# Kernel optimization log

Hardware: AMD Instinct MI355X
Metric: run time of the kernel (lower is better)

The kernel has to match this reference:

```python
import jax, jax.numpy as jnp
import numpy as np

# RT-DETR matcher hyperparameters (from config)
ALPHA, GAMMA = 0.25, 2.0
C_CLASS, C_BBOX, C_GIOU = 2.0, 5.0, 2.0
B, Q, C, T = 32, 300, 80, 100  # batch, queries, classes, targets-per-image


def _center_to_corners(b):
    cx, cy, w, h = jnp.split(b, 4, axis=-1)
    return jnp.concatenate([cx - 0.5 * w, cy - 0.5 * h, cx + 0.5 * w, cy + 0.5 * h], axis=-1)


def _generalized_box_iou(boxes1, boxes2):
    # boxes1 [N,4], boxes2 [M,4] in corner format -> [N,M] GIoU
    area1 = (boxes1[:, 2] - boxes1[:, 0]) * (boxes1[:, 3] - boxes1[:, 1])
    area2 = (boxes2[:, 2] - boxes2[:, 0]) * (boxes2[:, 3] - boxes2[:, 1])
    lt = jnp.maximum(boxes1[:, None, :2], boxes2[None, :, :2])
    rb = jnp.minimum(boxes1[:, None, 2:], boxes2[None, :, 2:])
    wh = jnp.clip(rb - lt, 0.0)
    inter = wh[..., 0] * wh[..., 1]
    union = area1[:, None] + area2[None, :] - inter
    iou = inter / union
    lt_e = jnp.minimum(boxes1[:, None, :2], boxes2[None, :, :2])
    rb_e = jnp.maximum(boxes1[:, None, 2:], boxes2[None, :, 2:])
    wh_e = jnp.clip(rb_e - lt_e, 0.0)
    enclose = wh_e[..., 0] * wh_e[..., 1]
    return iou - (enclose - union) / enclose


def setup_inputs() -> dict:
    key = jax.random.key(0)
    k1, k2, k3, k4 = jax.random.split(key, 4)
    logits = jax.random.normal(k1, (B, Q, C), dtype=jnp.float32)
    pred_boxes = jax.random.uniform(k2, (B, Q, 4), dtype=jnp.float32)
    target_labels = jax.random.randint(k3, (B * T,), 0, C)
    target_boxes = jax.random.uniform(k4, (B * T, 4), dtype=jnp.float32)
    return {"logits": logits, "pred_boxes": pred_boxes,
            "target_labels": target_labels, "target_boxes": target_boxes}


def reference(logits, pred_boxes, target_labels, target_boxes):
    batch_size, num_queries, num_classes = logits.shape
    out_bbox = pred_boxes.reshape(-1, 4)                      # [B*Q, 4]
    # focal-style class cost (use_focal_loss=True)
    out_prob = jax.nn.sigmoid(logits.reshape(-1, num_classes))  # [B*Q, C]
    out_prob = out_prob[:, target_labels]                       # [B*Q, B*T]
    neg_cost = (1 - ALPHA) * out_prob ** GAMMA * -jnp.log(1 - out_prob + 1e-8)
    pos_cost = ALPHA * (1 - out_prob) ** GAMMA * -jnp.log(out_prob + 1e-8)
    class_cost = pos_cost - neg_cost
    # pairwise L1 cost on cxcywh boxes
    bbox_cost = jnp.sum(jnp.abs(out_bbox[:, None, :] - target_boxes[None, :, :]), axis=-1)
    # pairwise GIoU cost on corner boxes
    giou_cost = -_generalized_box_iou(_center_to_corners(out_bbox), _center_to_corners(target_boxes))
    cost_matrix = C_BBOX * bbox_cost + C_CLASS * class_cost + C_GIOU * giou_cost
    return cost_matrix.reshape(batch_size, num_queries, -1)    # [B, Q, B*T]
```

## Files before the change

kernel.cpp:

```cpp
#include <hip/hip_runtime.h>


constexpr int BB = 32, QQ = 300, CN = 80, TT = 100;
constexpr int NQ = BB * QQ;
constexpr int NT = BB * TT;
constexpr int JQ = NT / 4;

__global__ __launch_bounds__(256) void class_cost_kernel(
    const float* __restrict__ logits, float* __restrict__ cc2, int n) {
  int idx = blockIdx.x * blockDim.x + threadIdx.x;
  if (idx >= n) return;
  float x = logits[idx];
  float p = 1.0f / (1.0f + expf(-x));
  float neg = 0.75f * p * p * (-logf(1.0f - p + 1e-8f));
  float pos = 0.25f * (1.0f - p) * (1.0f - p) * (-logf(p + 1e-8f));
  cc2[idx] = 2.0f * (pos - neg);
}

template <bool USE_TABLE>
__global__ __launch_bounds__(256) void pair_kernel(
    const float4* __restrict__ pred_boxes,
    const float4* __restrict__ target_boxes,
    const int4*   __restrict__ labels4,
    const float*  __restrict__ cc2,
    const float*  __restrict__ logits,
    float4*       __restrict__ out)
{
  int tid = blockIdx.x * blockDim.x + threadIdx.x;
  if (tid >= NQ * JQ) return;
  int i  = tid / JQ;
  int jq = tid - i * JQ;

  float4 p = pred_boxes[i];
  float px0 = p.x - 0.5f * p.z, py0 = p.y - 0.5f * p.w;
  float px1 = p.x + 0.5f * p.z, py1 = p.y + 0.5f * p.w;
  float pa  = (px1 - px0) * (py1 - py0);

  int4 lab = labels4[jq];
  const int* labp = &lab.x;
  const float* ccrow = USE_TABLE ? (cc2 + i * CN) : nullptr;
  const float* lgrow = USE_TABLE ? nullptr : (logits + i * CN);

  float res[4];
#pragma unroll
  for (int k = 0; k < 4; ++k) {
    float4 t = target_boxes[jq * 4 + k];
    float l1 = fabsf(p.x - t.x) + fabsf(p.y - t.y) +
               fabsf(p.z - t.z) + fabsf(p.w - t.w);
    float tx0 = t.x - 0.5f * t.z, ty0 = t.y - 0.5f * t.w;
    float tx1 = t.x + 0.5f * t.z, ty1 = t.y + 0.5f * t.w;
    float ta  = (tx1 - tx0) * (ty1 - ty0);
    float ltx = fmaxf(px0, tx0), lty = fmaxf(py0, ty0);
    float rbx = fminf(px1, tx1), rby = fminf(py1, ty1);
    float iw = fmaxf(rbx - ltx, 0.0f), ih = fmaxf(rby - lty, 0.0f);
    float inter = iw * ih;
    float uni = pa + ta - inter;
    float iou = inter / uni;
    float ex0 = fminf(px0, tx0), ey0 = fminf(py0, ty0);
    float ex1 = fmaxf(px1, tx1), ey1 = fmaxf(py1, ty1);
    float ew = fmaxf(ex1 - ex0, 0.0f), eh = fmaxf(ey1 - ey0, 0.0f);
    float enc = ew * eh;
    float giou = iou - (enc - uni) / enc;

    int l = labp[k];
    float cls;
    if (USE_TABLE) {
      cls = ccrow[l];
    } else {
      float x = lgrow[l];
      float pr = 1.0f / (1.0f + expf(-x));
      float neg = 0.75f * pr * pr * (-logf(1.0f - pr + 1e-8f));
      float pos = 0.25f * (1.0f - pr) * (1.0f - pr) * (-logf(pr + 1e-8f));
      cls = 2.0f * (pos - neg);
    }
    res[k] = 5.0f * l1 + cls - 2.0f * giou;
  }
  out[tid] = make_float4(res[0], res[1], res[2], res[3]);
}

extern "C" void kernel_launch(void* const* d_in, const int* in_sizes, int n_in,
                              void* d_out, int out_size, void* d_ws, size_t ws_size,
                              hipStream_t stream) {
  const float*  logits = (const float*)d_in[0];
  const float4* pred   = (const float4*)d_in[1];
  const int4*   labels = (const int4*)d_in[2];
  const float4* tboxes = (const float4*)d_in[3];
  float4* out = (float4*)d_out;

  size_t need = (size_t)NQ * CN * sizeof(float);
  int pair_threads = NQ * JQ;
  int pair_blocks = (pair_threads + 255) / 256;

  if (ws_size >= need) {
    float* cc2 = (float*)d_ws;
    int n = NQ * CN;
    class_cost_kernel<<<(n + 255) / 256, 256, 0, stream>>>(logits, cc2, n);
    pair_kernel<true><<<pair_blocks, 256, 0, stream>>>(
        pred, tboxes, labels, cc2, logits, out);
  } else {
    pair_kernel<false><<<pair_blocks, 256, 0, stream>>>(
        pred, tboxes, labels, nullptr, logits, out);
  }
}
```

Baseline: 171.7 us.

## Tile pair kernel over 32-row chunks, keep target data in registers, use fast reciprocals

Restructures the pair kernel onto a 2D grid. Each thread owns four targets, precomputes their corners, areas and labels once, then loops over 32 prediction rows staged in shared memory. This removes the per-element integer divide and the repeated target loads and corner math. It also replaces the IEEE divisions with the hardware approximate reciprocal and drops the clamp on the enclosing width and height. That changes numerics slightly, and the grid is small (4 stripes by 300 row chunks), which may limit occupancy.

```diff
diff --git a/kernel.cpp b/kernel.cpp
--- a/kernel.cpp
+++ b/kernel.cpp
@@ -4,7 +4,9 @@
 constexpr int BB = 32, QQ = 300, CN = 80, TT = 100;
 constexpr int NQ = BB * QQ;
 constexpr int NT = BB * TT;
-constexpr int JQ = NT / 4;
+constexpr int JG = NT / 4;
+constexpr int RCHUNK = 32;
+constexpr int STRIPES = (JG + 255) / 256;
 
 __global__ __launch_bounds__(256) void class_cost_kernel(
     const float* __restrict__ logits, float* __restrict__ cc2, int n) {
@@ -17,65 +19,126 @@
   cc2[idx] = 2.0f * (pos - neg);
 }
 
-template <bool USE_TABLE>
-__global__ __launch_bounds__(256) void pair_kernel(
+__global__ __launch_bounds__(256, 4) void pair_kernel(
     const float4* __restrict__ pred_boxes,
     const float4* __restrict__ target_boxes,
-    const int4*   __restrict__ labels4,
+    const int*    __restrict__ labels,
     const float*  __restrict__ cc2,
+    float4*       __restrict__ out)
+{
+  const int tid  = threadIdx.x;
+  const int jg   = blockIdx.x * 256 + tid;
+  const int row0 = blockIdx.y * RCHUNK;
+
+  __shared__ float4 s_pred[RCHUNK];
+  if (tid < RCHUNK) s_pred[tid] = pred_boxes[row0 + tid];
+  __syncthreads();
+  if (jg >= JG) return;
+
+  float tcx[4], tcy[4], tw[4], th[4];
+  float tx0[4], ty0[4], tx1[4], ty1[4], ta[4];
+  int   loff[4];
+#pragma unroll
+  for (int k = 0; k < 4; ++k) {
+    float4 t = target_boxes[jg * 4 + k];
+    tcx[k] = t.x; tcy[k] = t.y; tw[k] = t.z; th[k] = t.w;
+    tx0[k] = t.x - 0.5f * t.z;  ty0[k] = t.y - 0.5f * t.w;
+    tx1[k] = t.x + 0.5f * t.z;  ty1[k] = t.y + 0.5f * t.w;
+    ta[k]  = (tx1[k] - tx0[k]) * (ty1[k] - ty0[k]);
+    loff[k] = labels[jg * 4 + k];
+  }
+
+  const size_t outbase = (size_t)jg;
+  for (int r = 0; r < RCHUNK; ++r) {
+    const int i = row0 + r;
+    float4 p = s_pred[r];
+    float px0 = p.x - 0.5f * p.z, py0 = p.y - 0.5f * p.w;
+    float px1 = p.x + 0.5f * p.z, py1 = p.y + 0.5f * p.w;
+    float pa  = (px1 - px0) * (py1 - py0);
+    const float* ccrow = cc2 + (size_t)i * CN;
+
+    float res[4];
+#pragma unroll
+    for (int k = 0; k < 4; ++k) {
+      float l1 = fabsf(p.x - tcx[k]) + fabsf(p.y - tcy[k]) +
+                 fabsf(p.z - tw[k])  + fabsf(p.w - th[k]);
+      float ltx = fmaxf(px0, tx0[k]), lty = fmaxf(py0, ty0[k]);
+      float rbx = fminf(px1, tx1[k]), rby = fminf(py1, ty1[k]);
+      float iw = fmaxf(rbx - ltx, 0.0f), ih = fmaxf(rby - lty, 0.0f);
+      float inter = iw * ih;
+      float uni = pa + ta[k] - inter;
+      float iou = inter * __builtin_amdgcn_rcpf(uni);
+      float ex0 = fminf(px0, tx0[k]), ey0 = fminf(py0, ty0[k]);
+      float ex1 = fmaxf(px1, tx1[k]), ey1 = fmaxf(py1, ty1[k]);
+      float enc = (ex1 - ex0) * (ey1 - ey0);
+      float giou = iou - (enc - uni) * __builtin_amdgcn_rcpf(enc);
+      res[k] = 5.0f * l1 + ccrow[loff[k]] - 2.0f * giou;
+    }
+    out[(size_t)i * JG + outbase] = make_float4(res[0], res[1], res[2], res[3]);
+  }
+}
+
+__global__ __launch_bounds__(256, 4) void pair_kernel_nows(
+    const float4* __restrict__ pred_boxes,
+    const float4* __restrict__ target_boxes,
+    const int*    __restrict__ labels,
     const float*  __restrict__ logits,
     float4*       __restrict__ out)
 {
-  int tid = blockIdx.x * blockDim.x + threadIdx.x;
-  if (tid >= NQ * JQ) return;
-  int i  = tid / JQ;
-  int jq = tid - i * JQ;
+  const int tid  = threadIdx.x;
+  const int jg   = blockIdx.x * 256 + tid;
+  const int row0 = blockIdx.y * RCHUNK;
 
-  float4 p = pred_boxes[i];
-  float px0 = p.x - 0.5f * p.z, py0 = p.y - 0.5f * p.w;
-  float px1 = p.x + 0.5f * p.z, py1 = p.y + 0.5f * p.w;
-  float pa  = (px1 - px0) * (py1 - py0);
+  __shared__ float4 s_pred[RCHUNK];
+  if (tid < RCHUNK) s_pred[tid] = pred_boxes[row0 + tid];
+  __syncthreads();
+  if (jg >= JG) return;
 
-  int4 lab = labels4[jq];
-  const int* labp = &lab.x;
-  const float* ccrow = USE_TABLE ? (cc2 + i * CN) : nullptr;
-  const float* lgrow = USE_TABLE ? nullptr : (logits + i * CN);
-
-  float res[4];
+  float tcx[4], tcy[4], tw[4], th[4];
+  float tx0[4], ty0[4], tx1[4], ty1[4], ta[4];
+  int   loff[4];
 #pragma unroll
   for (int k = 0; k < 4; ++k) {
-    float4 t = target_boxes[jq * 4 + k];
-    float l1 = fabsf(p.x - t.x) + fabsf(p.y - t.y) +
-               fabsf(p.z - t.z) + fabsf(p.w - t.w);
-    float tx0 = t.x - 0.5f * t.z, ty0 = t.y - 0.5f * t.w;
-    float tx1 = t.x + 0.5f * t.z, ty1 = t.y + 0.5f * t.w;
-    float ta  = (tx1 - tx0) * (ty1 - ty0);
-    float ltx = fmaxf(px0, tx0), lty = fmaxf(py0, ty0);
-    float rbx = fminf(px1, tx1), rby = fminf(py1, ty1);
-    float iw = fmaxf(rbx - ltx, 0.0f), ih = fmaxf(rby - lty, 0.0f);
-    float inter = iw * ih;
-    float uni = pa + ta - inter;
-    float iou = inter / uni;
-    float ex0 = fminf(px0, tx0), ey0 = fminf(py0, ty0);
-    float ex1 = fmaxf(px1, tx1), ey1 = fmaxf(py1, ty1);
-    float ew = fmaxf(ex1 - ex0, 0.0f), eh = fmaxf(ey1 - ey0, 0.0f);
-    float enc = ew * eh;
-    float giou = iou - (enc - uni) / enc;
+    float4 t = target_boxes[jg * 4 + k];
+    tcx[k] = t.x; tcy[k] = t.y; tw[k] = t.z; th[k] = t.w;
+    tx0[k] = t.x - 0.5f * t.z;  ty0[k] = t.y - 0.5f * t.w;
+    tx1[k] = t.x + 0.5f * t.z;  ty1[k] = t.y + 0.5f * t.w;
+    ta[k]  = (tx1[k] - tx0[k]) * (ty1[k] - ty0[k]);
+    loff[k] = labels[jg * 4 + k];
+  }
 
-    int l = labp[k];
-    float cls;
-    if (USE_TABLE) {
-      cls = ccrow[l];
-    } else {
-      float x = lgrow[l];
+  for (int r = 0; r < RCHUNK; ++r) {
+    const int i = row0 + r;
+    float4 p = s_pred[r];
+    float px0 = p.x - 0.5f * p.z, py0 = p.y - 0.5f * p.w;
+    float px1 = p.x + 0.5f * p.z, py1 = p.y + 0.5f * p.w;
+    float pa  = (px1 - px0) * (py1 - py0);
+    const float* lgrow = logits + (size_t)i * CN;
+
+    float res[4];
+#pragma unroll
+    for (int k = 0; k < 4; ++k) {
+      float l1 = fabsf(p.x - tcx[k]) + fabsf(p.y - tcy[k]) +
+                 fabsf(p.z - tw[k])  + fabsf(p.w - th[k]);
+      float ltx = fmaxf(px0, tx0[k]), lty = fmaxf(py0, ty0[k]);
+      float rbx = fminf(px1, tx1[k]), rby = fminf(py1, ty1[k]);
+      float iw = fmaxf(rbx - ltx, 0.0f), ih = fmaxf(rby - lty, 0.0f);
+      float inter = iw * ih;
+      float uni = pa + ta[k] - inter;
+      float iou = inter * __builtin_amdgcn_rcpf(uni);
+      float ex0 = fminf(px0, tx0[k]), ey0 = fminf(py0, ty0[k]);
+      float ex1 = fmaxf(px1, tx1[k]), ey1 = fmaxf(py1, ty1[k]);
+      float enc = (ex1 - ex0) * (ey1 - ey0);
+      float giou = iou - (enc - uni) * __builtin_amdgcn_rcpf(enc);
+
+      float x = lgrow[loff[k]];
       float pr = 1.0f / (1.0f + expf(-x));
       float neg = 0.75f * pr * pr * (-logf(1.0f - pr + 1e-8f));
       float pos = 0.25f * (1.0f - pr) * (1.0f - pr) * (-logf(pr + 1e-8f));
-      cls = 2.0f * (pos - neg);
+      res[k] = 5.0f * l1 + 2.0f * (pos - neg) - 2.0f * giou;
     }
-    res[k] = 5.0f * l1 + cls - 2.0f * giou;
+    out[(size_t)i * JG + jg] = make_float4(res[0], res[1], res[2], res[3]);
   }
-  out[tid] = make_float4(res[0], res[1], res[2], res[3]);
 }
 
 extern "C" void kernel_launch(void* const* d_in, const int* in_sizes, int n_in,
@@ -83,22 +146,19 @@
                               hipStream_t stream) {
   const float*  logits = (const float*)d_in[0];
   const float4* pred   = (const float4*)d_in[1];
-  const int4*   labels = (const int4*)d_in[2];
+  const int*    labels = (const int*)d_in[2];
   const float4* tboxes = (const float4*)d_in[3];
   float4* out = (float4*)d_out;
 
-  size_t need = (size_t)NQ * CN * sizeof(float);
-  int pair_threads = NQ * JQ;
-  int pair_blocks = (pair_threads + 255) / 256;
+  const size_t need = (size_t)NQ * CN * sizeof(float);
+  dim3 grid(STRIPES, NQ / RCHUNK);
 
   if (ws_size >= need) {
     float* cc2 = (float*)d_ws;
     int n = NQ * CN;
     class_cost_kernel<<<(n + 255) / 256, 256, 0, stream>>>(logits, cc2, n);
-    pair_kernel<true><<<pair_blocks, 256, 0, stream>>>(
-        pred, tboxes, labels, cc2, logits, out);
+    pair_kernel<<<grid, 256, 0, stream>>>(pred, tboxes, labels, cc2, out);
   } else {
-    pair_kernel<false><<<pair_blocks, 256, 0, stream>>>(
-        pred, tboxes, labels, nullptr, logits, out);
+    pair_kernel_nows<<<grid, 256, 0, stream>>>(pred, tboxes, labels, logits, out);
   }
 }
```

Result: faster. 162.8 us (-5.2%).
